# Performance work log

Measured on AMD Instinct MI355X. Metric: run time of the kernel, lower is better.

The kernel has to match this reference:

```python
import jax, jax.numpy as jnp
import numpy as np

V, F, H, W, K, B, J = 50000, 100000, 256, 256, 1, 4, 256

def setup_inputs() -> dict:
    key = jax.random.key(0)
    ks = jax.random.split(key, 8)
    pix_to_face = jax.random.randint(ks[0], (1, H, W, K), 0, F, dtype=jnp.int32)
    bary = jax.random.uniform(ks[1], (1, H, W, K, 3), dtype=jnp.float32)
    bary = bary / jnp.sum(bary, axis=-1, keepdims=True)  # valid barycentric weights
    faces = jax.random.randint(ks[2], (F, 3), 0, V, dtype=jnp.int32)
    verts = jax.random.normal(ks[3], (V, 3), dtype=jnp.float32)
    vertex_normals = jax.random.normal(ks[4], (V, 3), dtype=jnp.float32)
    directions = jax.random.normal(ks[5], (B, J, 3), dtype=jnp.float32)
    directions = directions / jnp.linalg.norm(directions, axis=-1, keepdims=True)
    env_colors = jax.random.uniform(ks[6], (B, J, 3), dtype=jnp.float32)  # environment_map * sineweight
    texels = jax.random.uniform(ks[7], (1, H, W, 3), dtype=jnp.float32)
    return {"pix_to_face": pix_to_face, "bary_coords": bary, "faces": faces,
            "verts": verts, "vertex_normals": vertex_normals,
            "directions": directions, "env_colors": env_colors, "texels": texels}

def reference(pix_to_face, bary_coords, faces, verts, vertex_normals, directions, env_colors, texels):
    # interpolate_face_attributes: gather per-face vertex normals, bary-weighted sum
    faces_normals = vertex_normals[faces]                     # (F, 3verts, 3)
    attr = faces_normals[pix_to_face]                         # (1, H, W, K, 3verts, 3)
    pixel_normals = jnp.einsum('nhwkv,nhwkvc->nhwkc', bary_coords, attr)[:, :, :, 0, :]  # (1,H,W,3)
    # F.normalize(p=2, dim=-1, eps=1e-6): divide by clamped norm
    norm = jnp.maximum(jnp.linalg.norm(pixel_normals, axis=-1, keepdims=True), 1e-6)
    pixel_normals = pixel_normals / norm
    normals = jnp.broadcast_to(pixel_normals, (directions.shape[0],) + pixel_normals.shape[1:])  # (B,H,W,3)
    # diffuse dot products over all J lights, clamped to [0,1]
    diffuse = jnp.clip(jnp.einsum('bhwc,bjc->bhwj', normals, directions), 0.0, 1.0)  # (B,H,W,J)
    diffuse = jnp.einsum('bjc,bhwj->bhwc', env_colors, diffuse)                      # (B,H,W,3)
    colors = diffuse * texels
    return colors, diffuse, texels, normals
```

## Files before the change

kernel.cpp:

```cpp
#include <hip/hip_runtime.h>

#define NPIX  65536
#define BB    4
#define JJ    256


struct F3 { float x, y, z; };
struct I3 { int x, y, z; };

__global__ __launch_bounds__(256, 8) void shade_kernel(
    const int*   __restrict__ p2f,
    const float* __restrict__ bary,
    const int*   __restrict__ faces,
    const float* __restrict__ vnorm,
    const float* __restrict__ dirs,
    const float* __restrict__ env,
    const float* __restrict__ tex,
    float*       __restrict__ out)
{
    const int b     = blockIdx.x >> 9;
    const int pbase = (blockIdx.x & 511) << 7;
    const int t     = threadIdx.x;
    const int i     = t & 63;
    const int jq    = __builtin_amdgcn_readfirstlane(t >> 6);

    __shared__ float nlds[128][3];
    __shared__ float part[4][128][3];

    const F3* __restrict__ bary3  = (const F3*)bary;
    const I3* __restrict__ faces3 = (const I3*)faces;
    const F3* __restrict__ vn3    = (const F3*)vnorm;
    const F3* __restrict__ tex3   = (const F3*)tex;

    if (t < 128) {
        const int p = pbase + t;
        const int f = p2f[p];
        const I3 vv = faces3[f];
        const F3 bc = bary3[p];
        const F3 a0 = vn3[vv.x];
        const F3 a1 = vn3[vv.y];
        const F3 a2 = vn3[vv.z];
        float nx = bc.x*a0.x + bc.y*a1.x + bc.z*a2.x;
        float ny = bc.x*a0.y + bc.y*a1.y + bc.z*a2.y;
        float nz = bc.x*a0.z + bc.y*a1.z + bc.z*a2.z;
        const float inv = 1.0f / fmaxf(sqrtf(nx*nx + ny*ny + nz*nz), 1e-6f);
        nx *= inv; ny *= inv; nz *= inv;
        nlds[t][0] = nx; nlds[t][1] = ny; nlds[t][2] = nz;

        float* __restrict__ nor = out + (3*BB*NPIX*2 + 3*NPIX);
        const int o = 3*(b*NPIX + p);
        nor[o+0] = nx; nor[o+1] = ny; nor[o+2] = nz;

        if (b == 0) {
            const F3 tv = tex3[p];
            float* __restrict__ tx = out + 3*BB*NPIX*2;
            tx[3*p+0] = tv.x; tx[3*p+1] = tv.y; tx[3*p+2] = tv.z;
        }
    }
    __syncthreads();

    const float n0x = nlds[i][0],    n0y = nlds[i][1],    n0z = nlds[i][2];
    const float n1x = nlds[64+i][0], n1y = nlds[64+i][1], n1z = nlds[64+i][2];

    float a0r=0.f, a0g=0.f, a0b=0.f, a1r=0.f, a1g=0.f, a1b=0.f;
    const float* __restrict__ dp = dirs + b*(JJ*3) + jq*(64*3);
    const float* __restrict__ ep = env  + b*(JJ*3) + jq*(64*3);

    #pragma unroll 8
    for (int j = 0; j < 64; ++j) {
        const float dx = dp[3*j+0], dy = dp[3*j+1], dz = dp[3*j+2];
        const float er = ep[3*j+0], eg = ep[3*j+1], eb = ep[3*j+2];
        float w0 = fmaf(n0z, dz, fmaf(n0y, dy, n0x*dx));
        float w1 = fmaf(n1z, dz, fmaf(n1y, dy, n1x*dx));
        w0 = fminf(fmaxf(w0, 0.f), 1.f);
        w1 = fminf(fmaxf(w1, 0.f), 1.f);
        a0r = fmaf(er, w0, a0r); a0g = fmaf(eg, w0, a0g); a0b = fmaf(eb, w0, a0b);
        a1r = fmaf(er, w1, a1r); a1g = fmaf(eg, w1, a1g); a1b = fmaf(eb, w1, a1b);
    }

    const int w = t >> 6;
    part[w][i][0]    = a0r; part[w][i][1]    = a0g; part[w][i][2]    = a0b;
    part[w][64+i][0] = a1r; part[w][64+i][1] = a1g; part[w][64+i][2] = a1b;
    __syncthreads();

    if (t < 128) {
        const int p = pbase + t;
        const float sr = part[0][t][0]+part[1][t][0]+part[2][t][0]+part[3][t][0];
        const float sg = part[0][t][1]+part[1][t][1]+part[2][t][1]+part[3][t][1];
        const float sb = part[0][t][2]+part[1][t][2]+part[2][t][2]+part[3][t][2];

        const F3 tv = tex3[p];
        const int o = 3*(b*NPIX + p);
        out[o+0] = sr*tv.x; out[o+1] = sg*tv.y; out[o+2] = sb*tv.z;

        float* __restrict__ dif = out + 3*BB*NPIX;
        dif[o+0] = sr; dif[o+1] = sg; dif[o+2] = sb;
    }
}

extern "C" void kernel_launch(void* const* d_in, const int* in_sizes, int n_in,
                              void* d_out, int out_size, void* d_ws, size_t ws_size,
                              hipStream_t stream) {
    const int*   p2f   = (const int*)  d_in[0];
    const float* bary  = (const float*)d_in[1];
    const int*   faces = (const int*)  d_in[2];
    const float* vnorm = (const float*)d_in[4];
    const float* dirs  = (const float*)d_in[5];
    const float* env   = (const float*)d_in[6];
    const float* tex   = (const float*)d_in[7];
    float* out = (float*)d_out;

    const int grid = BB * (NPIX / 128);
    shade_kernel<<<grid, 256, 0, stream>>>(
        p2f, bary, faces, vnorm, dirs, env, tex, out);
}
```

Before: 19.72 us.

## Stage light directions and colors in LDS as float4 and spread normal gathers across waves

Each block now loads its batch's 256 directions and env colors into LDS packed as two float4 per light. The inner loop reads these with wide LDS loads instead of scalar global loads. The per-pixel normal gather is split so each of the four waves handles 32 pixels, rather than two waves doing all 128 while the others sit idle. Normals are stored as float4 in LDS and the unroll factor is raised. The cost is extra LDS capacity plus a per-block staging load of the light data.

Result: slower. 40.28 us (+104.2%).

```diff
diff --git a/kernel.cpp b/kernel.cpp
--- a/kernel.cpp
+++ b/kernel.cpp
@@ -22,19 +22,28 @@
     const int pbase = (blockIdx.x & 511) << 7;
     const int t     = threadIdx.x;
     const int i     = t & 63;
-    const int jq    = __builtin_amdgcn_readfirstlane(t >> 6);
+    const int w     = t >> 6;
 
-    __shared__ float nlds[128][3];
-    __shared__ float part[4][128][3];
+    __shared__ float4 llds[JJ][2];
+    __shared__ float4 nlds[128];
+    __shared__ float  part[4][128][3];
 
     const F3* __restrict__ bary3  = (const F3*)bary;
     const I3* __restrict__ faces3 = (const I3*)faces;
     const F3* __restrict__ vn3    = (const F3*)vnorm;
     const F3* __restrict__ tex3   = (const F3*)tex;
 
-    if (t < 128) {
-        const int p = pbase + t;
-        const int f = p2f[p];
+    {
+        const F3 d = ((const F3*)dirs)[b * JJ + t];
+        const F3 e = ((const F3*)env )[b * JJ + t];
+        llds[t][0] = make_float4(d.x, d.y, d.z, e.x);
+        llds[t][1] = make_float4(e.y, e.z, 0.f, 0.f);
+    }
+
+    if (i < 32) {
+        const int lp = (w << 5) + i;
+        const int p  = pbase + lp;
+        const int f  = p2f[p];
         const I3 vv = faces3[f];
         const F3 bc = bary3[p];
         const F3 a0 = vn3[vv.x];
@@ -45,7 +54,7 @@
         float nz = bc.x*a0.z + bc.y*a1.z + bc.z*a2.z;
         const float inv = 1.0f / fmaxf(sqrtf(nx*nx + ny*ny + nz*nz), 1e-6f);
         nx *= inv; ny *= inv; nz *= inv;
-        nlds[t][0] = nx; nlds[t][1] = ny; nlds[t][2] = nz;
+        nlds[lp] = make_float4(nx, ny, nz, 0.f);
 
         float* __restrict__ nor = out + (3*BB*NPIX*2 + 3*NPIX);
         const int o = 3*(b*NPIX + p);
@@ -59,28 +68,26 @@
     }
     __syncthreads();
 
-    const float n0x = nlds[i][0],    n0y = nlds[i][1],    n0z = nlds[i][2];
-    const float n1x = nlds[64+i][0], n1y = nlds[64+i][1], n1z = nlds[64+i][2];
+    const float4 n0 = nlds[i];
+    const float4 n1 = nlds[64 + i];
 
     float a0r=0.f, a0g=0.f, a0b=0.f, a1r=0.f, a1g=0.f, a1b=0.f;
-    const float* __restrict__ dp = dirs + b*(JJ*3) + jq*(64*3);
-    const float* __restrict__ ep = env  + b*(JJ*3) + jq*(64*3);
+    const int jb = w << 6;
 
-    #pragma unroll 8
+    #pragma unroll 16
     for (int j = 0; j < 64; ++j) {
-        const float dx = dp[3*j+0], dy = dp[3*j+1], dz = dp[3*j+2];
-        const float er = ep[3*j+0], eg = ep[3*j+1], eb = ep[3*j+2];
-        float w0 = fmaf(n0z, dz, fmaf(n0y, dy, n0x*dx));
-        float w1 = fmaf(n1z, dz, fmaf(n1y, dy, n1x*dx));
+        const float4 q0 = llds[jb + j][0];
+        const float4 q1 = llds[jb + j][1];
+        float w0 = fmaf(n0.z, q0.z, fmaf(n0.y, q0.y, n0.x*q0.x));
+        float w1 = fmaf(n1.z, q0.z, fmaf(n1.y, q0.y, n1.x*q0.x));
         w0 = fminf(fmaxf(w0, 0.f), 1.f);
         w1 = fminf(fmaxf(w1, 0.f), 1.f);
-        a0r = fmaf(er, w0, a0r); a0g = fmaf(eg, w0, a0g); a0b = fmaf(eb, w0, a0b);
-        a1r = fmaf(er, w1, a1r); a1g = fmaf(eg, w1, a1g); a1b = fmaf(eb, w1, a1b);
+        a0r = fmaf(q0.w, w0, a0r); a0g = fmaf(q1.x, w0, a0g); a0b = fmaf(q1.y, w0, a0b);
+        a1r = fmaf(q0.w, w1, a1r); a1g = fmaf(q1.x, w1, a1g); a1b = fmaf(q1.y, w1, a1b);
     }
 
-    const int w = t >> 6;
-    part[w][i][0]    = a0r; part[w][i][1]    = a0g; part[w][i][2]    = a0b;
-    part[w][64+i][0] = a1r; part[w][64+i][1] = a1g; part[w][64+i][2] = a1b;
+    part[w][i][0]      = a0r; part[w][i][1]      = a0g; part[w][i][2]      = a0b;
+    part[w][64+i][0]   = a1r; part[w][64+i][1]   = a1g; part[w][64+i][2]   = a1b;
     __syncthreads();
 
     if (t < 128) {
```

## Use 512-thread blocks, 4 pixels per lane, and readlane-broadcast lights

Applied to the files above, without the earlier changes.

Blocks grow to 512 threads covering 256 pixels. Each of 8 waves handles 32 lights, and each lane accumulates 4 pixels. Light directions and colors are loaded once per lane and broadcast with readlane instead of repeated scalar or global loads. LDS uses float4 rows, which makes the 8-way partial reduction vectorized. This raises FMA work per load and removes per-iteration memory traffic for the lights, at the cost of more registers and fewer, larger blocks.

After: 22.86 us. 1.16x slower.

```diff
diff --git a/kernel.cpp b/kernel.cpp
--- a/kernel.cpp
+++ b/kernel.cpp
@@ -8,7 +8,7 @@
 struct F3 { float x, y, z; };
 struct I3 { int x, y, z; };
 
-__global__ __launch_bounds__(256, 8) void shade_kernel(
+__global__ __launch_bounds__(512, 8) void shade_kernel(
     const int*   __restrict__ p2f,
     const float* __restrict__ bary,
     const int*   __restrict__ faces,
@@ -18,21 +18,29 @@
     const float* __restrict__ tex,
     float*       __restrict__ out)
 {
-    const int b     = blockIdx.x >> 9;
-    const int pbase = (blockIdx.x & 511) << 7;
+    const int b     = blockIdx.x >> 8;
+    const int pbase = (blockIdx.x & 255) << 8;
     const int t     = threadIdx.x;
-    const int i     = t & 63;
-    const int jq    = __builtin_amdgcn_readfirstlane(t >> 6);
+    const int lane  = t & 63;
+    const int w     = t >> 6;
 
-    __shared__ float nlds[128][3];
-    __shared__ float part[4][128][3];
+    __shared__ float4 nlds[256];
+    __shared__ float4 part4[8][256];
 
     const F3* __restrict__ bary3  = (const F3*)bary;
     const I3* __restrict__ faces3 = (const I3*)faces;
     const F3* __restrict__ vn3    = (const F3*)vnorm;
     const F3* __restrict__ tex3   = (const F3*)tex;
 
-    if (t < 128) {
+    float ldx = 0.f, ldy = 0.f, ldz = 0.f, ler = 0.f, leg = 0.f, leb = 0.f;
+    if (lane < 32) {
+        const int j = b * JJ + (w << 5) + lane;
+        const F3 d = ((const F3*)dirs)[j];
+        const F3 e = ((const F3*)env )[j];
+        ldx = d.x; ldy = d.y; ldz = d.z; ler = e.x; leg = e.y; leb = e.z;
+    }
+
+    if (t < 256) {
         const int p = pbase + t;
         const int f = p2f[p];
         const I3 vv = faces3[f];
@@ -45,7 +53,7 @@
         float nz = bc.x*a0.z + bc.y*a1.z + bc.z*a2.z;
         const float inv = 1.0f / fmaxf(sqrtf(nx*nx + ny*ny + nz*nz), 1e-6f);
         nx *= inv; ny *= inv; nz *= inv;
-        nlds[t][0] = nx; nlds[t][1] = ny; nlds[t][2] = nz;
+        nlds[t] = make_float4(nx, ny, nz, 0.f);
 
         float* __restrict__ nor = out + (3*BB*NPIX*2 + 3*NPIX);
         const int o = 3*(b*NPIX + p);
@@ -59,42 +67,51 @@
     }
     __syncthreads();
 
-    const float n0x = nlds[i][0],    n0y = nlds[i][1],    n0z = nlds[i][2];
-    const float n1x = nlds[64+i][0], n1y = nlds[64+i][1], n1z = nlds[64+i][2];
-
-    float a0r=0.f, a0g=0.f, a0b=0.f, a1r=0.f, a1g=0.f, a1b=0.f;
-    const float* __restrict__ dp = dirs + b*(JJ*3) + jq*(64*3);
-    const float* __restrict__ ep = env  + b*(JJ*3) + jq*(64*3);
-
-    #pragma unroll 8
-    for (int j = 0; j < 64; ++j) {
-        const float dx = dp[3*j+0], dy = dp[3*j+1], dz = dp[3*j+2];
-        const float er = ep[3*j+0], eg = ep[3*j+1], eb = ep[3*j+2];
-        float w0 = fmaf(n0z, dz, fmaf(n0y, dy, n0x*dx));
-        float w1 = fmaf(n1z, dz, fmaf(n1y, dy, n1x*dx));
-        w0 = fminf(fmaxf(w0, 0.f), 1.f);
-        w1 = fminf(fmaxf(w1, 0.f), 1.f);
-        a0r = fmaf(er, w0, a0r); a0g = fmaf(eg, w0, a0g); a0b = fmaf(eb, w0, a0b);
-        a1r = fmaf(er, w1, a1r); a1g = fmaf(eg, w1, a1g); a1b = fmaf(eb, w1, a1b);
+    float nX[4], nY[4], nZ[4], aR[4], aG[4], aB[4];
+    #pragma unroll
+    for (int k = 0; k < 4; ++k) {
+        const float4 n = nlds[(k << 6) + lane];
+        nX[k] = n.x; nY[k] = n.y; nZ[k] = n.z;
+        aR[k] = 0.f; aG[k] = 0.f; aB[k] = 0.f;
     }
 
-    const int w = t >> 6;
-    part[w][i][0]    = a0r; part[w][i][1]    = a0g; part[w][i][2]    = a0b;
-    part[w][64+i][0] = a1r; part[w][64+i][1] = a1g; part[w][64+i][2] = a1b;
+    #pragma unroll
+    for (int j = 0; j < 32; ++j) {
+        const float dx = __int_as_float(__builtin_amdgcn_readlane(__float_as_int(ldx), j));
+        const float dy = __int_as_float(__builtin_amdgcn_readlane(__float_as_int(ldy), j));
+        const float dz = __int_as_float(__builtin_amdgcn_readlane(__float_as_int(ldz), j));
+        const float er = __int_as_float(__builtin_amdgcn_readlane(__float_as_int(ler), j));
+        const float eg = __int_as_float(__builtin_amdgcn_readlane(__float_as_int(leg), j));
+        const float eb = __int_as_float(__builtin_amdgcn_readlane(__float_as_int(leb), j));
+        #pragma unroll
+        for (int k = 0; k < 4; ++k) {
+            float wgt = fmaf(nZ[k], dz, fmaf(nY[k], dy, nX[k]*dx));
+            wgt = fminf(fmaxf(wgt, 0.f), 1.f);
+            aR[k] = fmaf(er, wgt, aR[k]);
+            aG[k] = fmaf(eg, wgt, aG[k]);
+            aB[k] = fmaf(eb, wgt, aB[k]);
+        }
+    }
+
+    #pragma unroll
+    for (int k = 0; k < 4; ++k)
+        part4[w][(k << 6) + lane] = make_float4(aR[k], aG[k], aB[k], 0.f);
     __syncthreads();
 
-    if (t < 128) {
+    if (t < 256) {
+        float4 s = part4[0][t];
+        #pragma unroll
+        for (int q = 1; q < 8; ++q) {
+            const float4 v = part4[q][t];
+            s.x += v.x; s.y += v.y; s.z += v.z;
+        }
         const int p = pbase + t;
-        const float sr = part[0][t][0]+part[1][t][0]+part[2][t][0]+part[3][t][0];
-        const float sg = part[0][t][1]+part[1][t][1]+part[2][t][1]+part[3][t][1];
-        const float sb = part[0][t][2]+part[1][t][2]+part[2][t][2]+part[3][t][2];
-
         const F3 tv = tex3[p];
         const int o = 3*(b*NPIX + p);
-        out[o+0] = sr*tv.x; out[o+1] = sg*tv.y; out[o+2] = sb*tv.z;
+        out[o+0] = s.x*tv.x; out[o+1] = s.y*tv.y; out[o+2] = s.z*tv.z;
 
         float* __restrict__ dif = out + 3*BB*NPIX;
-        dif[o+0] = sr; dif[o+1] = sg; dif[o+2] = sb;
+        dif[o+0] = s.x; dif[o+1] = s.y; dif[o+2] = s.z;
     }
 }
 
@@ -110,7 +127,7 @@
     const float* tex   = (const float*)d_in[7];
     float* out = (float*)d_out;
 
-    const int grid = BB * (NPIX / 128);
-    shade_kernel<<<grid, 256, 0, stream>>>(
+    const int grid = BB * (NPIX / 256);
+    shade_kernel<<<grid, 512, 0, stream>>>(
         p2f, bary, faces, vnorm, dirs, env, tex, out);
 }
```

## Split lights into two halves per pixel and reduce partials in registers

Applied to the files above, without the earlier changes.

Each thread now handles one pixel across half the lights (128), where before it handled two pixels across a quarter (64). The reduction becomes one LDS write by the upper half plus an add in the lower half, replacing a four-way LDS partial sum. Normals are stored as float4 in LDS, and the clamp to 1 is dropped because unit normals dotted with unit directions cannot exceed 1. This trades reuse of each direction/env load across two pixels for less LDS traffic and a shorter reduction, and the loop is twice as long per thread.

Result: slower. 21.52 us (+9.1%).

```diff
diff --git a/kernel.cpp b/kernel.cpp
--- a/kernel.cpp
+++ b/kernel.cpp
@@ -22,18 +22,20 @@
     const int pbase = (blockIdx.x & 511) << 7;
     const int t     = threadIdx.x;
     const int i     = t & 63;
-    const int jq    = __builtin_amdgcn_readfirstlane(t >> 6);
+    const int w     = t >> 6;
+    const int jh    = __builtin_amdgcn_readfirstlane(w >> 1);
+    const int q     = ((w & 1) << 6) | i;
 
-    __shared__ float nlds[128][3];
-    __shared__ float part[4][128][3];
+    __shared__ float4 nlds[128];
+    __shared__ float  part[128][3];
 
     const F3* __restrict__ bary3  = (const F3*)bary;
     const I3* __restrict__ faces3 = (const I3*)faces;
     const F3* __restrict__ vn3    = (const F3*)vnorm;
     const F3* __restrict__ tex3   = (const F3*)tex;
 
-    if (t < 128) {
-        const int p = pbase + t;
+    if (jh == 0) {
+        const int p = pbase + q;
         const int f = p2f[p];
         const I3 vv = faces3[f];
         const F3 bc = bary3[p];
@@ -45,7 +47,7 @@
         float nz = bc.x*a0.z + bc.y*a1.z + bc.z*a2.z;
         const float inv = 1.0f / fmaxf(sqrtf(nx*nx + ny*ny + nz*nz), 1e-6f);
         nx *= inv; ny *= inv; nz *= inv;
-        nlds[t][0] = nx; nlds[t][1] = ny; nlds[t][2] = nz;
+        nlds[q] = make_float4(nx, ny, nz, 0.f);
 
         float* __restrict__ nor = out + (3*BB*NPIX*2 + 3*NPIX);
         const int o = 3*(b*NPIX + p);
@@ -59,36 +61,31 @@
     }
     __syncthreads();
 
-    const float n0x = nlds[i][0],    n0y = nlds[i][1],    n0z = nlds[i][2];
-    const float n1x = nlds[64+i][0], n1y = nlds[64+i][1], n1z = nlds[64+i][2];
-
-    float a0r=0.f, a0g=0.f, a0b=0.f, a1r=0.f, a1g=0.f, a1b=0.f;
-    const float* __restrict__ dp = dirs + b*(JJ*3) + jq*(64*3);
-    const float* __restrict__ ep = env  + b*(JJ*3) + jq*(64*3);
+    const float4 n = nlds[q];
+    float ar = 0.f, ag = 0.f, ab = 0.f;
+    const float* __restrict__ dp = dirs + b*(JJ*3) + jh*(128*3);
+    const float* __restrict__ ep = env  + b*(JJ*3) + jh*(128*3);
 
     #pragma unroll 8
-    for (int j = 0; j < 64; ++j) {
+    for (int j = 0; j < 128; ++j) {
         const float dx = dp[3*j+0], dy = dp[3*j+1], dz = dp[3*j+2];
         const float er = ep[3*j+0], eg = ep[3*j+1], eb = ep[3*j+2];
-        float w0 = fmaf(n0z, dz, fmaf(n0y, dy, n0x*dx));
-        float w1 = fmaf(n1z, dz, fmaf(n1y, dy, n1x*dx));
-        w0 = fminf(fmaxf(w0, 0.f), 1.f);
-        w1 = fminf(fmaxf(w1, 0.f), 1.f);
-        a0r = fmaf(er, w0, a0r); a0g = fmaf(eg, w0, a0g); a0b = fmaf(eb, w0, a0b);
-        a1r = fmaf(er, w1, a1r); a1g = fmaf(eg, w1, a1g); a1b = fmaf(eb, w1, a1b);
+        float wgt = fmaf(n.z, dz, fmaf(n.y, dy, n.x*dx));
+        wgt = fmaxf(wgt, 0.f);
+        ar = fmaf(er, wgt, ar); ag = fmaf(eg, wgt, ag); ab = fmaf(eb, wgt, ab);
     }
 
-    const int w = t >> 6;
-    part[w][i][0]    = a0r; part[w][i][1]    = a0g; part[w][i][2]    = a0b;
-    part[w][64+i][0] = a1r; part[w][64+i][1] = a1g; part[w][64+i][2] = a1b;
+    if (jh == 1) {
+        part[q][0] = ar; part[q][1] = ag; part[q][2] = ab;
+    }
     __syncthreads();
 
-    if (t < 128) {
-        const int p = pbase + t;
-        const float sr = part[0][t][0]+part[1][t][0]+part[2][t][0]+part[3][t][0];
-        const float sg = part[0][t][1]+part[1][t][1]+part[2][t][1]+part[3][t][1];
-        const float sb = part[0][t][2]+part[1][t][2]+part[2][t][2]+part[3][t][2];
+    if (jh == 0) {
+        const float sr = ar + part[q][0];
+        const float sg = ag + part[q][1];
+        const float sb = ab + part[q][2];
 
+        const int p = pbase + q;
         const F3 tv = tex3[p];
         const int o = 3*(b*NPIX + p);
         out[o+0] = sr*tv.x; out[o+1] = sg*tv.y; out[o+2] = sb*tv.z;
```
